# Performance work log

Measured on AMD Instinct MI355X. Metric: run time of the kernel, lower is better.

The kernel has to match this reference:

```python
import jax, jax.numpy as jnp
import numpy as np

TEMP = 34.0   # Dynamic_conv2d default temperature
EPS = 1e-5    # BatchNorm eps


def setup_inputs() -> dict:
    key = jax.random.key(0)
    ks = jax.random.split(key, 4)
    B, Cin, Cout, H, W, K = 8, 32, 16, 256, 256, 4
    hidden = int(Cin * 0.25) + 1  # attention2d hidden planes = 9
    return {
        "x": jax.random.normal(ks[0], (B, Cin, H, W), jnp.float32),
        "weight": jax.random.normal(ks[1], (K, Cout, Cin, 3, 3), jnp.float32) * 0.05,
        "bias": jnp.zeros((K, Cout), jnp.float32),
        "fc1_w": jax.random.normal(ks[2], (hidden, Cin), jnp.float32) * 0.1,
        "fc2_w": jax.random.normal(ks[3], (K, hidden), jnp.float32) * 0.1,
        "fc2_b": jnp.zeros((K,), jnp.float32),
        "bn_gamma": jnp.ones((Cout,), jnp.float32),
        "bn_beta": jnp.zeros((Cout,), jnp.float32),
        "bn_mean": jnp.zeros((Cout,), jnp.float32),
        "bn_var": jnp.ones((Cout,), jnp.float32),
    }


def reference(x, weight, bias, fc1_w, fc2_w, fc2_b, bn_gamma, bn_beta, bn_mean, bn_var):
    xu = jnp.repeat(jnp.repeat(x, 2, axis=2), 2, axis=3)  # [B, Cin, 2H, 2W]

    # 2) attention over K kernels: global avg pool -> 1x1 conv -> relu -> 1x1 conv -> softmax(logits/T)
    pooled = xu.mean(axis=(2, 3))                          # [B, Cin]
    h = jax.nn.relu(pooled @ fc1_w.T)                      # [B, hidden]
    logits = h @ fc2_w.T + fc2_b                           # [B, K]
    attn = jax.nn.softmax(logits / TEMP, axis=-1)          # [B, K]

    # 3) per-sample aggregated conv weights & bias (CondConv-style)
    agg_w = jnp.einsum('bk,koihw->boihw', attn, weight)    # [B, Cout, Cin, 3, 3]
    agg_b = attn @ bias                                    # [B, Cout]

    # 4) per-sample 3x3 conv, stride 1, padding 1 (vmap instead of grouped-conv trick)
    dn = jax.lax.conv_dimension_numbers((1,) + xu.shape[1:], agg_w.shape[1:],
                                        ('NCHW', 'OIHW', 'NCHW'))
    def conv_one(xi, wi, bi):
        y = jax.lax.conv_general_dilated(xi[None], wi, window_strides=(1, 1),
                                         padding=((1, 1), (1, 1)),
                                         dimension_numbers=dn)[0]
        return y + bi[:, None, None]
    y = jax.vmap(conv_one)(xu, agg_w, agg_b)               # [B, Cout, 2H, 2W]

    # 5) BatchNorm (inference with running stats) + ReLU
    scale = bn_gamma / jnp.sqrt(bn_var + EPS)
    shift = bn_beta - bn_mean * scale
    return jax.nn.relu(y * scale[:, None, None] + shift[:, None, None])
```

## Files before the change

kernel.cpp:

```cpp
#include <hip/hip_runtime.h>
#include <hip/hip_bf16.h>

#define B_  8
#define CIN 32
#define COUT 16
#define K_  4
#define HID 9
#define HIN 256
#define WIN 256
#define HW  (HIN * WIN)
#define HOUT 512
#define WOUT 512
#define TEMP 34.0f
#define EPS_ 1e-5f

#define SLAB 1168

typedef float f32x4 __attribute__((ext_vector_type(4)));
typedef __fp16 fp16x2 __attribute__((ext_vector_type(2)));
typedef __fp16 f16x8 __attribute__((ext_vector_type(8)));

union FragB { unsigned u[4]; f16x8 h; };

__device__ inline unsigned pk2(float a, float b) {
    union { fp16x2 f; unsigned u; } x;
    x.f = __builtin_amdgcn_cvt_pkrtz(a, b);
    return x.u;
}
__device__ inline unsigned short f16b(float v) {
    union { __fp16 h; unsigned short u; } x;
    x.h = (__fp16)v;
    return x.u;
}

__global__ __launch_bounds__(1024) void pool_kernel(const float* __restrict__ x,
                                                    float* __restrict__ pooled) {
    int bc = blockIdx.x;
    const float4* p = (const float4*)(x + (size_t)bc * HW);
    float s = 0.f;
    for (int i = threadIdx.x; i < HW / 4; i += 1024) {
        float4 v = p[i];
        s += v.x + v.y + v.z + v.w;
    }
    #pragma unroll
    for (int off = 32; off > 0; off >>= 1) s += __shfl_down(s, off);
    __shared__ float red[16];
    if ((threadIdx.x & 63) == 0) red[threadIdx.x >> 6] = s;
    __syncthreads();
    if (threadIdx.x < 16) {
        float t = red[threadIdx.x];
        t += __shfl_down(t, 8);
        t += __shfl_down(t, 4);
        t += __shfl_down(t, 2);
        t += __shfl_down(t, 1);
        if (threadIdx.x == 0) pooled[bc] = t * (1.f / HW);
    }
}

__global__ __launch_bounds__(256) void attn_weights_kernel(
    const float* __restrict__ pooled, const float* __restrict__ weight,
    const float* __restrict__ bias, const float* __restrict__ fc1_w,
    const float* __restrict__ fc2_w, const float* __restrict__ fc2_b,
    const float* __restrict__ gamma, const float* __restrict__ beta,
    const float* __restrict__ mean, const float* __restrict__ var,
    unsigned short* __restrict__ wpk16, float* __restrict__ bias_eff) {
    int b = blockIdx.x;
    __shared__ float attn[K_];
    if (threadIdx.x == 0) {
        const float* pb = pooled + b * CIN;
        float h[HID];
        for (int j = 0; j < HID; ++j) {
            float s = 0.f;
            for (int c = 0; c < CIN; ++c) s += pb[c] * fc1_w[j * CIN + c];
            h[j] = fmaxf(s, 0.f);
        }
        float lg[K_];
        float mx = -1e30f;
        for (int k = 0; k < K_; ++k) {
            float s = fc2_b[k];
            for (int j = 0; j < HID; ++j) s += h[j] * fc2_w[k * HID + j];
            lg[k] = s * (1.f / TEMP);
            mx = fmaxf(mx, lg[k]);
        }
        float den = 0.f;
        for (int k = 0; k < K_; ++k) { lg[k] = expf(lg[k] - mx); den += lg[k]; }
        for (int k = 0; k < K_; ++k) attn[k] = lg[k] / den;
    }
    __syncthreads();
    float a0 = attn[0], a1 = attn[1], a2 = attn[2], a3v = attn[3];

    for (int p = threadIdx.x; p < COUT * CIN; p += 256) {
        int o = p >> 5, i = p & 31;
        float scale = gamma[o] / sqrtf(var[o] + EPS_);
        const float* w0 = weight + ((size_t)(0 * COUT + o) * CIN + i) * 9;
        const int kstr = COUT * CIN * 9;
        float a3w[9];
        #pragma unroll
        for (int t = 0; t < 9; ++t)
            a3w[t] = scale * (a0 * w0[t] + a1 * w0[kstr + t] +
                              a2 * w0[2 * kstr + t] + a3v * w0[3 * kstr + t]);
        float tmp[2][2][3];
        #pragma unroll
        for (int kx = 0; kx < 3; ++kx) {
            tmp[0][0][kx] = a3w[0 * 3 + kx];
            tmp[0][1][kx] = a3w[1 * 3 + kx] + a3w[2 * 3 + kx];
            tmp[1][0][kx] = a3w[0 * 3 + kx] + a3w[1 * 3 + kx];
            tmp[1][1][kx] = a3w[2 * 3 + kx];
        }
        float w16[16];
        #pragma unroll
        for (int py = 0; py < 2; ++py)
            #pragma unroll
            for (int px = 0; px < 2; ++px)
                #pragma unroll
                for (int u = 0; u < 2; ++u)
                    #pragma unroll
                    for (int v = 0; v < 2; ++v) {
                        const float* t = tmp[py][u];
                        float val = (px == 0) ? (v == 0 ? t[0] : t[1] + t[2])
                                              : (v == 0 ? t[0] + t[1] : t[2]);
                        w16[(py * 2 + px) * 4 + u * 2 + v] = val;
                    }
        const int ks = i >> 3, g = (i >> 1) & 3, hf = i & 1;
        const int l = g * 16 + o;
        #pragma unroll
        for (int par = 0; par < 4; ++par)
            #pragma unroll
            for (int d = 0; d < 4; ++d)
                wpk16[(((size_t)(b * 16 + par * 4 + ks) * 64 + l) * 4 + d) * 2 +
                      hf] = f16b(w16[par * 4 + d]);
    }
    if (threadIdx.x < COUT) {
        int o = threadIdx.x;
        float scale = gamma[o] / sqrtf(var[o] + EPS_);
        float shift = beta[o] - mean[o] * scale;
        float s = a0 * bias[0 * COUT + o] + a1 * bias[1 * COUT + o] +
                  a2 * bias[2 * COUT + o] + a3v * bias[3 * COUT + o];
        bias_eff[b * COUT + o] = s * scale + shift;
    }
}

__global__ __launch_bounds__(256) void conv_kernel(
    const float* __restrict__ x, const unsigned* __restrict__ wpk,
    const float* __restrict__ bias_eff, float* __restrict__ out) {
    const int tile = blockIdx.x;
    const int b = blockIdx.y;
    const int r0 = (tile >> 3) * 32, c0 = (tile & 7) * 32;
    const int tid = threadIdx.x;

    __shared__ unsigned lds32[16 * SLAB];

    const int w = tid >> 6, lane = tid & 63;
    const int g = lane >> 4, n = lane & 15;

    const float* xb = x + (size_t)b * CIN * HW;

    #pragma unroll
    for (int i2 = 0; i2 < 16; ++i2) {
        const float* p0 = xb + (size_t)(2 * i2) * HW;
        #pragma unroll
        for (int t = 0; t < 5; ++t) {
            int e = tid + t * 256;
            bool live = e < 34 * 34;
            int pr = e / 34, pc = e - pr * 34;
            int gr = r0 - 1 + pr, gc = c0 - 1 + pc;
            bool ok = live & ((unsigned)gr < (unsigned)HIN) &
                      ((unsigned)gc < (unsigned)WIN);
            int off = ok ? (gr * WIN + gc) : 0;
            float v0 = p0[off];
            float v1 = p0[off + HW];
            if (!ok) { v0 = 0.f; v1 = 0.f; }
            if (live) lds32[i2 * SLAB + e] = pk2(v0, v1);
        }
    }

    f16x8 areg[4][4];
    {
        const f16x8* wp = (const f16x8*)wpk + (size_t)b * 1024 + lane;
        #pragma unroll
        for (int par = 0; par < 4; ++par)
            #pragma unroll
            for (int ks = 0; ks < 4; ++ks)
                areg[par][ks] = wp[(par * 4 + ks) * 64];
    }
    float bias4[4];
    #pragma unroll
    for (int q = 0; q < 4; ++q) bias4[q] = bias_eff[b * COUT + g * 4 + q];

    __syncthreads();

    for (int h = 0; h < 2; ++h) {
        #pragma unroll
        for (int p2 = 0; p2 < 4; ++p2) {
            const int rA = w * 8 + p2 * 2;

            f32x4 acc[2][4];
            #pragma unroll
            for (int rr = 0; rr < 2; ++rr)
                #pragma unroll
                for (int par = 0; par < 4; ++par)
                    acc[rr][par] = (f32x4){0.f, 0.f, 0.f, 0.f};

            #pragma unroll
            for (int ks = 0; ks < 4; ++ks) {
                const int base = (ks * 4 + g) * SLAB + rA * 34 + (h << 4) + n;
                unsigned nb[4][3];
                #pragma unroll
                for (int rr = 0; rr < 4; ++rr)
                    #pragma unroll
                    for (int dv = 0; dv < 3; ++dv)
                        nb[rr][dv] = lds32[base + rr * 34 + dv];
                #pragma unroll
                for (int rr = 0; rr < 2; ++rr)
                    #pragma unroll
                    for (int par = 0; par < 4; ++par) {
                        const int py = par >> 1, px = par & 1;
                        FragB bf;
                        bf.u[0] = nb[rr + py][px];
                        bf.u[1] = nb[rr + py][px + 1];
                        bf.u[2] = nb[rr + py + 1][px];
                        bf.u[3] = nb[rr + py + 1][px + 1];
                        acc[rr][par] = __builtin_amdgcn_mfma_f32_16x16x32_f16(
                            areg[par][ks], bf.h, acc[rr][par], 0, 0, 0);
                    }
            }

            #pragma unroll
            for (int rr = 0; rr < 2; ++rr) {
                #pragma unroll
                for (int py = 0; py < 2; ++py) {
                    const int y = 2 * (r0 + rA + rr) + py;
                    #pragma unroll
                    for (int q = 0; q < 4; ++q) {
                        float2 st;
                        st.x = fmaxf(acc[rr][2 * py + 0][q] + bias4[q], 0.f);
                        st.y = fmaxf(acc[rr][2 * py + 1][q] + bias4[q], 0.f);
                        *(float2*)&out[((size_t)(b * COUT + g * 4 + q) * HOUT +
                                        y) * WOUT +
                                       2 * (c0 + (h << 4) + n)] = st;
                    }
                }
            }
        }
    }
}

extern "C" void kernel_launch(void* const* d_in, const int* in_sizes, int n_in,
                              void* d_out, int out_size, void* d_ws, size_t ws_size,
                              hipStream_t stream) {
    const float* x      = (const float*)d_in[0];
    const float* weight = (const float*)d_in[1];
    const float* bias   = (const float*)d_in[2];
    const float* fc1_w  = (const float*)d_in[3];
    const float* fc2_w  = (const float*)d_in[4];
    const float* fc2_b  = (const float*)d_in[5];
    const float* bn_g   = (const float*)d_in[6];
    const float* bn_b   = (const float*)d_in[7];
    const float* bn_m   = (const float*)d_in[8];
    const float* bn_v   = (const float*)d_in[9];
    float* out = (float*)d_out;

    float* ws = (float*)d_ws;
    float*    pooled   = ws;
    float*    bias_eff = ws + 256;
    unsigned* wpk      = (unsigned*)(ws + 512);

    pool_kernel<<<dim3(B_ * CIN), dim3(1024), 0, stream>>>(x, pooled);
    attn_weights_kernel<<<dim3(B_), dim3(256), 0, stream>>>(
        pooled, weight, bias, fc1_w, fc2_w, fc2_b, bn_g, bn_b, bn_m, bn_v,
        (unsigned short*)wpk, bias_eff);
    conv_kernel<<<dim3(64, B_), dim3(256), 0, stream>>>(
        x, wpk, bias_eff, out);
}
```

Before: 81.64 us.

## Fuse pooling, attention and conv into one kernel with grid-wide barrier

Merges the pooling, attention/weight-aggregation and conv kernels into a single launch. Each block computes partial channel sums while it stages its input tile into LDS, then all 512 blocks meet at an atomic-counter grid barrier before every block reduces the partials and builds its own fp16 weight fragments in registers. This drops the separate full read of x for pooling and two extra launches. In exchange, every block redundantly recomputes the attention MLP and aggregated weights, and correctness depends on all 512 blocks being co-resident, since the spin-wait only has a bounded guard.

```diff
diff --git a/kernel.cpp b/kernel.cpp
--- a/kernel.cpp
+++ b/kernel.cpp
@@ -13,6 +13,8 @@
 #define WOUT 512
 #define TEMP 34.0f
 #define EPS_ 1e-5f
+#define KSTR (COUT * CIN * 9)
+#define NBLK 512
 
 #define SLAB 1168
 
@@ -27,142 +29,34 @@
     x.f = __builtin_amdgcn_cvt_pkrtz(a, b);
     return x.u;
 }
-__device__ inline unsigned short f16b(float v) {
-    union { __fp16 h; unsigned short u; } x;
-    x.h = (__fp16)v;
-    return x.u;
-}
-
-__global__ __launch_bounds__(1024) void pool_kernel(const float* __restrict__ x,
-                                                    float* __restrict__ pooled) {
-    int bc = blockIdx.x;
-    const float4* p = (const float4*)(x + (size_t)bc * HW);
-    float s = 0.f;
-    for (int i = threadIdx.x; i < HW / 4; i += 1024) {
-        float4 v = p[i];
-        s += v.x + v.y + v.z + v.w;
-    }
-    #pragma unroll
-    for (int off = 32; off > 0; off >>= 1) s += __shfl_down(s, off);
-    __shared__ float red[16];
-    if ((threadIdx.x & 63) == 0) red[threadIdx.x >> 6] = s;
-    __syncthreads();
-    if (threadIdx.x < 16) {
-        float t = red[threadIdx.x];
-        t += __shfl_down(t, 8);
-        t += __shfl_down(t, 4);
-        t += __shfl_down(t, 2);
-        t += __shfl_down(t, 1);
-        if (threadIdx.x == 0) pooled[bc] = t * (1.f / HW);
-    }
-}
-
-__global__ __launch_bounds__(256) void attn_weights_kernel(
-    const float* __restrict__ pooled, const float* __restrict__ weight,
+
+__global__ __launch_bounds__(256, 2) void fused_kernel(
+    const float* __restrict__ x, const float* __restrict__ weight,
     const float* __restrict__ bias, const float* __restrict__ fc1_w,
     const float* __restrict__ fc2_w, const float* __restrict__ fc2_b,
     const float* __restrict__ gamma, const float* __restrict__ beta,
     const float* __restrict__ mean, const float* __restrict__ var,
-    unsigned short* __restrict__ wpk16, float* __restrict__ bias_eff) {
-    int b = blockIdx.x;
-    __shared__ float attn[K_];
-    if (threadIdx.x == 0) {
-        const float* pb = pooled + b * CIN;
-        float h[HID];
-        for (int j = 0; j < HID; ++j) {
-            float s = 0.f;
-            for (int c = 0; c < CIN; ++c) s += pb[c] * fc1_w[j * CIN + c];
-            h[j] = fmaxf(s, 0.f);
-        }
-        float lg[K_];
-        float mx = -1e30f;
-        for (int k = 0; k < K_; ++k) {
-            float s = fc2_b[k];
-            for (int j = 0; j < HID; ++j) s += h[j] * fc2_w[k * HID + j];
-            lg[k] = s * (1.f / TEMP);
-            mx = fmaxf(mx, lg[k]);
-        }
-        float den = 0.f;
-        for (int k = 0; k < K_; ++k) { lg[k] = expf(lg[k] - mx); den += lg[k]; }
-        for (int k = 0; k < K_; ++k) attn[k] = lg[k] / den;
-    }
-    __syncthreads();
-    float a0 = attn[0], a1 = attn[1], a2 = attn[2], a3v = attn[3];
-
-    for (int p = threadIdx.x; p < COUT * CIN; p += 256) {
-        int o = p >> 5, i = p & 31;
-        float scale = gamma[o] / sqrtf(var[o] + EPS_);
-        const float* w0 = weight + ((size_t)(0 * COUT + o) * CIN + i) * 9;
-        const int kstr = COUT * CIN * 9;
-        float a3w[9];
-        #pragma unroll
-        for (int t = 0; t < 9; ++t)
-            a3w[t] = scale * (a0 * w0[t] + a1 * w0[kstr + t] +
-                              a2 * w0[2 * kstr + t] + a3v * w0[3 * kstr + t]);
-        float tmp[2][2][3];
-        #pragma unroll
-        for (int kx = 0; kx < 3; ++kx) {
-            tmp[0][0][kx] = a3w[0 * 3 + kx];
-            tmp[0][1][kx] = a3w[1 * 3 + kx] + a3w[2 * 3 + kx];
-            tmp[1][0][kx] = a3w[0 * 3 + kx] + a3w[1 * 3 + kx];
-            tmp[1][1][kx] = a3w[2 * 3 + kx];
-        }
-        float w16[16];
-        #pragma unroll
-        for (int py = 0; py < 2; ++py)
-            #pragma unroll
-            for (int px = 0; px < 2; ++px)
-                #pragma unroll
-                for (int u = 0; u < 2; ++u)
-                    #pragma unroll
-                    for (int v = 0; v < 2; ++v) {
-                        const float* t = tmp[py][u];
-                        float val = (px == 0) ? (v == 0 ? t[0] : t[1] + t[2])
-                                              : (v == 0 ? t[0] + t[1] : t[2]);
-                        w16[(py * 2 + px) * 4 + u * 2 + v] = val;
-                    }
-        const int ks = i >> 3, g = (i >> 1) & 3, hf = i & 1;
-        const int l = g * 16 + o;
-        #pragma unroll
-        for (int par = 0; par < 4; ++par)
-            #pragma unroll
-            for (int d = 0; d < 4; ++d)
-                wpk16[(((size_t)(b * 16 + par * 4 + ks) * 64 + l) * 4 + d) * 2 +
-                      hf] = f16b(w16[par * 4 + d]);
-    }
-    if (threadIdx.x < COUT) {
-        int o = threadIdx.x;
-        float scale = gamma[o] / sqrtf(var[o] + EPS_);
-        float shift = beta[o] - mean[o] * scale;
-        float s = a0 * bias[0 * COUT + o] + a1 * bias[1 * COUT + o] +
-                  a2 * bias[2 * COUT + o] + a3v * bias[3 * COUT + o];
-        bias_eff[b * COUT + o] = s * scale + shift;
-    }
-}
-
-__global__ __launch_bounds__(256) void conv_kernel(
-    const float* __restrict__ x, const unsigned* __restrict__ wpk,
-    const float* __restrict__ bias_eff, float* __restrict__ out) {
+    float* __restrict__ partials, unsigned* __restrict__ ctr,
+    float* __restrict__ out) {
     const int tile = blockIdx.x;
     const int b = blockIdx.y;
     const int r0 = (tile >> 3) * 32, c0 = (tile & 7) * 32;
     const int tid = threadIdx.x;
 
     __shared__ unsigned lds32[16 * SLAB];
-
-    const int w = tid >> 6, lane = tid & 63;
-    const int g = lane >> 4, n = lane & 15;
+    __shared__ float pooledL[32];
 
     const float* xb = x + (size_t)b * CIN * HW;
 
-    #pragma unroll
-    for (int i2 = 0; i2 < 16; ++i2) {
+    {
+        const int i2 = tid >> 4, cl = tid & 15;
         const float* p0 = xb + (size_t)(2 * i2) * HW;
-        #pragma unroll
-        for (int t = 0; t < 5; ++t) {
-            int e = tid + t * 256;
-            bool live = e < 34 * 34;
-            int pr = e / 34, pc = e - pr * 34;
+        float s0 = 0.f, s1 = 0.f;
+        #pragma unroll
+        for (int k = 0; k < 73; ++k) {
+            int u = cl + (k << 4);
+            bool live = (u < 34 * 34);
+            int pr = u / 34, pc = u - pr * 34;
             int gr = r0 - 1 + pr, gc = c0 - 1 + pc;
             bool ok = live & ((unsigned)gr < (unsigned)HIN) &
                       ((unsigned)gc < (unsigned)WIN);
@@ -170,26 +64,135 @@
             float v0 = p0[off];
             float v1 = p0[off + HW];
             if (!ok) { v0 = 0.f; v1 = 0.f; }
-            if (live) lds32[i2 * SLAB + e] = pk2(v0, v1);
-        }
-    }
+            bool inr = live & (pr >= 1) & (pr <= 32) & (pc >= 1) & (pc <= 32);
+            if (inr) { s0 += v0; s1 += v1; }
+            if (live) lds32[i2 * SLAB + u] = pk2(v0, v1);
+        }
+        #pragma unroll
+        for (int d = 1; d < 16; d <<= 1) {
+            s0 += __shfl_xor(s0, d);
+            s1 += __shfl_xor(s1, d);
+        }
+        if (cl == 0) {
+            float* pp = partials + ((size_t)(b * 64 + tile) * 32 + 2 * i2);
+            pp[0] = s0;
+            pp[1] = s1;
+        }
+    }
+
+    __threadfence();
+    __syncthreads();
+    if (tid == 0) {
+        __hip_atomic_fetch_add(ctr, 1u, __ATOMIC_ACQ_REL,
+                               __HIP_MEMORY_SCOPE_AGENT);
+        int guard = 0;
+        while (__hip_atomic_load(ctr, __ATOMIC_ACQUIRE,
+                                 __HIP_MEMORY_SCOPE_AGENT) < NBLK &&
+               guard < (1 << 16)) {
+            __builtin_amdgcn_s_sleep(8);
+            ++guard;
+        }
+    }
+    __syncthreads();
+
+    if (tid < 32) {
+        const float* pp = partials + (size_t)b * 64 * 32 + tid;
+        float s = 0.f;
+        #pragma unroll 8
+        for (int t = 0; t < 64; ++t) s += pp[t * 32];
+        pooledL[tid] = s * (1.f / HW);
+    }
+    __syncthreads();
+
+    float a0, a1, a2, a3v;
+    {
+        float h[HID];
+        #pragma unroll
+        for (int j = 0; j < HID; ++j) {
+            float s = 0.f;
+            for (int c = 0; c < CIN; ++c) s += pooledL[c] * fc1_w[j * CIN + c];
+            h[j] = fmaxf(s, 0.f);
+        }
+        float lg[K_];
+        float mx = -1e30f;
+        #pragma unroll
+        for (int k = 0; k < K_; ++k) {
+            float s = fc2_b[k];
+            for (int j = 0; j < HID; ++j) s += h[j] * fc2_w[k * HID + j];
+            lg[k] = s * (1.f / TEMP);
+            mx = fmaxf(mx, lg[k]);
+        }
+        float den = 0.f;
+        #pragma unroll
+        for (int k = 0; k < K_; ++k) { lg[k] = expf(lg[k] - mx); den += lg[k]; }
+        a0 = lg[0] / den; a1 = lg[1] / den;
+        a2 = lg[2] / den; a3v = lg[3] / den;
+    }
+
+    const int w = tid >> 6, lane = tid & 63;
+    const int g = lane >> 4, n = lane & 15;
 
     f16x8 areg[4][4];
     {
-        const f16x8* wp = (const f16x8*)wpk + (size_t)b * 1024 + lane;
-        #pragma unroll
-        for (int par = 0; par < 4; ++par)
-            #pragma unroll
-            for (int ks = 0; ks < 4; ++ks)
-                areg[par][ks] = wp[(par * 4 + ks) * 64];
+        const int o = n;
+        const float scale = gamma[o] / sqrtf(var[o] + EPS_);
+        #pragma unroll
+        for (int ks = 0; ks < 4; ++ks) {
+            float w16h[2][16];
+            #pragma unroll
+            for (int hf = 0; hf < 2; ++hf) {
+                const int i = ks * 8 + g * 2 + hf;
+                const float* w0 = weight + ((size_t)o * CIN + i) * 9;
+                float a3w[9];
+                #pragma unroll
+                for (int t = 0; t < 9; ++t)
+                    a3w[t] = scale * (a0 * w0[t] + a1 * w0[KSTR + t] +
+                                      a2 * w0[2 * KSTR + t] +
+                                      a3v * w0[3 * KSTR + t]);
+                float tmp[2][2][3];
+                #pragma unroll
+                for (int kx = 0; kx < 3; ++kx) {
+                    tmp[0][0][kx] = a3w[0 * 3 + kx];
+                    tmp[0][1][kx] = a3w[1 * 3 + kx] + a3w[2 * 3 + kx];
+                    tmp[1][0][kx] = a3w[0 * 3 + kx] + a3w[1 * 3 + kx];
+                    tmp[1][1][kx] = a3w[2 * 3 + kx];
+                }
+                #pragma unroll
+                for (int py = 0; py < 2; ++py)
+                    #pragma unroll
+                    for (int px = 0; px < 2; ++px)
+                        #pragma unroll
+                        for (int u = 0; u < 2; ++u)
+                            #pragma unroll
+                            for (int v = 0; v < 2; ++v) {
+                                const float* t = tmp[py][u];
+                                float val = (px == 0)
+                                                ? (v == 0 ? t[0] : t[1] + t[2])
+                                                : (v == 0 ? t[0] + t[1] : t[2]);
+                                w16h[hf][(py * 2 + px) * 4 + u * 2 + v] = val;
+                            }
+            }
+            #pragma unroll
+            for (int par = 0; par < 4; ++par) {
+                FragB f;
+                #pragma unroll
+                for (int d = 0; d < 4; ++d)
+                    f.u[d] = pk2(w16h[0][par * 4 + d], w16h[1][par * 4 + d]);
+                areg[par][ks] = f.h;
+            }
+        }
     }
     float bias4[4];
     #pragma unroll
-    for (int q = 0; q < 4; ++q) bias4[q] = bias_eff[b * COUT + g * 4 + q];
-
-    __syncthreads();
-
-    for (int h = 0; h < 2; ++h) {
+    for (int q = 0; q < 4; ++q) {
+        const int oc = g * 4 + q;
+        float sc = gamma[oc] / sqrtf(var[oc] + EPS_);
+        bias4[q] = (a0 * bias[oc] + a1 * bias[COUT + oc] +
+                    a2 * bias[2 * COUT + oc] + a3v * bias[3 * COUT + oc]) * sc +
+                   beta[oc] - mean[oc] * sc;
+    }
+
+    for (int h2 = 0; h2 < 2; ++h2) {
         #pragma unroll
         for (int p2 = 0; p2 < 4; ++p2) {
             const int rA = w * 8 + p2 * 2;
@@ -203,7 +206,8 @@
 
             #pragma unroll
             for (int ks = 0; ks < 4; ++ks) {
-                const int base = (ks * 4 + g) * SLAB + rA * 34 + (h << 4) + n;
+                const int base =
+                    (ks * 4 + g) * SLAB + rA * 34 + (h2 << 4) + n;
                 unsigned nb[4][3];
                 #pragma unroll
                 for (int rr = 0; rr < 4; ++rr)
@@ -237,7 +241,7 @@
                         st.y = fmaxf(acc[rr][2 * py + 1][q] + bias4[q], 0.f);
                         *(float2*)&out[((size_t)(b * COUT + g * 4 + q) * HOUT +
                                         y) * WOUT +
-                                       2 * (c0 + (h << 4) + n)] = st;
+                                       2 * (c0 + (h2 << 4) + n)] = st;
                     }
                 }
             }
@@ -260,15 +264,12 @@
     const float* bn_v   = (const float*)d_in[9];
     float* out = (float*)d_out;
 
-    float* ws = (float*)d_ws;
-    float*    pooled   = ws;
-    float*    bias_eff = ws + 256;
-    unsigned* wpk      = (unsigned*)(ws + 512);
-
-    pool_kernel<<<dim3(B_ * CIN), dim3(1024), 0, stream>>>(x, pooled);
-    attn_weights_kernel<<<dim3(B_), dim3(256), 0, stream>>>(
-        pooled, weight, bias, fc1_w, fc2_w, fc2_b, bn_g, bn_b, bn_m, bn_v,
-        (unsigned short*)wpk, bias_eff);
-    conv_kernel<<<dim3(64, B_), dim3(256), 0, stream>>>(
-        x, wpk, bias_eff, out);
+    float*    partials = (float*)d_ws;
+    unsigned* ctr      = (unsigned*)d_ws + 16384;
+
+    hipMemsetAsync(ctr, 0, sizeof(unsigned), stream);
+
+    fused_kernel<<<dim3(64, B_), dim3(256), 0, stream>>>(
+        x, weight, bias, fc1_w, fc2_w, fc2_b, bn_g, bn_b, bn_m, bn_v,
+        partials, ctr, out);
 }
```

Result: slower. 186.5 us (+128.5%).
